# Performance work log

Hardware: AMD Instinct MI355X
Metric: run time of the kernel (lower is better)

Reference implementation:

```python
import jax, jax.numpy as jnp
import numpy as np

SHIFT = 1  # fixed realization of the random +/-1 shift_direction in __init__


def setup_inputs() -> dict:
    key = jax.random.key(0)
    k1, k2, k3 = jax.random.split(key, 3)
    x = jax.random.normal(k1, (1, 128, 56, 56), dtype=jnp.float32)
    w0 = jax.random.normal(k2, (32, 2, 3, 3), dtype=jnp.float32)   # weights[0]
    w1 = jax.random.normal(k3, (4, 64), dtype=jnp.float32)         # weights[1]
    return {"x": x, "w0": w0, "w1": w1}


def reference(x, w0, w1):
    # x: [1,128,56,56] -> [1,64,2,56,56]
    t3 = x.reshape(1, 64, 2, 56, 56)
    # 1x1 channel mix: contract the 64 axis with w1 [4,64]
    t4 = jnp.einsum('kjlmn,ij->kilmn', t3, w1)  # [1,4,2,56,56]
    # First unfold: kernel 3 along the last spatial axis (h2), zero pad 1.
    p1 = jnp.pad(t4, ((0, 0), (0, 0), (0, 0), (0, 0), (1, 1)))
    A = jnp.stack([p1[..., k:k + 56] for k in range(3)], axis=-2)  # [1,4,2,56,3,56]
    # Second unfold: kernel 3 along the SAME (already unfolded) position axis,
    # zero pad 1 applied to the unfolded tensor (matches torch's two-stage unfold).
    p2 = jnp.pad(A, ((0, 0), (0, 0), (0, 0), (0, 0), (0, 0), (1, 1)))
    B = jnp.stack([p2[..., k:k + 56] for k in range(3)], axis=-2)  # [1,4,2,56,3,3,56]
    # Contract group channel j=2 and both kernel offsets i,k with w0 [32,2,3,3]
    t6 = jnp.einsum('mpjoikn,ljik->mlpon', B, w0)  # [1,32,4,56,56]
    y = t6.reshape(1, 128, 56, 56)
    # Cyclic shift along H (axis 2)
    return jnp.roll(y, SHIFT, axis=2)
```

## Files before the change

### kernel.cpp

```cpp
#include <hip/hip_runtime.h>


__global__ __launch_bounds__(256) void fused_shift_unfold_kernel(
    const float* __restrict__ x,
    const float* __restrict__ w0,
    const float* __restrict__ w1,
    float* __restrict__ out)
{
    __shared__ float s_t4[2][60];
    __shared__ float s_w0[576];

    const int tid = threadIdx.x;
    const int h   = blockIdx.x;
    const int p   = blockIdx.y;
    const int o   = h ? h - 1 : 55;

    if (tid < 112) {
        const int j = (tid >= 56);
        const int n = tid - j * 56;
        const float* xp = x + j * 3136 + o * 56 + n;
        const float* wp = w1 + p * 64;
        float a0 = 0.f, a1 = 0.f, a2 = 0.f, a3 = 0.f;
        #pragma unroll
        for (int q = 0; q < 64; q += 4) {
            a0 += wp[q + 0] * xp[(q + 0) * 6272];
            a1 += wp[q + 1] * xp[(q + 1) * 6272];
            a2 += wp[q + 2] * xp[(q + 2) * 6272];
            a3 += wp[q + 3] * xp[(q + 3) * 6272];
        }
        s_t4[j][n + 2] = (a0 + a1) + (a2 + a3);
    } else {
        const int t = tid - 112;
        ((float4*)s_w0)[t] = ((const float4*)w0)[t];
        if (t < 8) {
            const int j   = t & 1;
            const int q2  = t >> 1;
            s_t4[j][q2 < 2 ? q2 : q2 + 56] = 0.f;
        }
    }
    __syncthreads();

    const int l = tid >> 3;
    const int b = tid & 7;

    float wreg[2][9];
    #pragma unroll
    for (int j = 0; j < 2; ++j)
        #pragma unroll
        for (int t = 0; t < 9; ++t)
            wreg[j][t] = s_w0[l * 18 + j * 9 + t];

    float* obase = out + (l * 4 + p) * 3136 + h * 56;
    #pragma unroll
    for (int i7 = 0; i7 < 7; ++i7) {
        const int n = b + i7 * 8;
        float acc = 0.f;
        #pragma unroll
        for (int k = 0; k < 3; ++k) {
            float s = 0.f;
            #pragma unroll
            for (int j = 0; j < 2; ++j) {
                const float* rp = &s_t4[j][n];
                s += wreg[j][0 + k] * rp[k + 0];
                s += wreg[j][3 + k] * rp[k + 1];
                s += wreg[j][6 + k] * rp[k + 2];
            }
            const int m = n + k - 1;
            acc += ((unsigned)m < 56u) ? s : 0.f;
        }
        obase[n] = acc;
    }
}

extern "C" void kernel_launch(void* const* d_in, const int* in_sizes, int n_in,
                              void* d_out, int out_size, void* d_ws, size_t ws_size,
                              hipStream_t stream) {
    (void)in_sizes; (void)n_in; (void)out_size; (void)d_ws; (void)ws_size;
    const float* x  = (const float*)d_in[0];
    const float* w0 = (const float*)d_in[1];
    const float* w1 = (const float*)d_in[2];
    float* out = (float*)d_out;

    dim3 grid(56, 4);
    fused_shift_unfold_kernel<<<grid, 256, 0, stream>>>(x, w0, w1, out);
}
```

Baseline: 59.37 us.

## Split channel reduction across thread pairs and vectorize output stores with float4

Doubles the block to 512 threads. Each 64-term channel reduction is now split across two lanes and combined with a shuffle, which halves the serial chain of strided global loads per thread. The output stage is reorganized so each thread computes 4 consecutive outputs from a register window and writes them with one float4 store, instead of 7 scalar stores. In exchange it adds a shuffle, leaves idle lanes (g>=14), and puts more threads per block.

Result: no change. 59.86 us (+0.8%).

```diff
diff --git a/kernel.cpp b/kernel.cpp
--- a/kernel.cpp
+++ b/kernel.cpp
@@ -1,7 +1,7 @@
 #include <hip/hip_runtime.h>
 
 
-__global__ __launch_bounds__(256) void fused_shift_unfold_kernel(
+__global__ __launch_bounds__(512) void fused_shift_unfold_kernel(
     const float* __restrict__ x,
     const float* __restrict__ w0,
     const float* __restrict__ w1,
@@ -15,60 +15,74 @@
     const int p   = blockIdx.y;
     const int o   = h ? h - 1 : 55;
 
-    if (tid < 112) {
-        const int j = (tid >= 56);
-        const int n = tid - j * 56;
-        const float* xp = x + j * 3136 + o * 56 + n;
-        const float* wp = w1 + p * 64;
+    if (tid < 224) {
+        const int v    = tid >> 1;
+        const int half = tid & 1;
+        const int j    = (v >= 56);
+        const int n    = v - j * 56;
+        const float* xp = x + j * 3136 + o * 56 + n + half * 32 * 6272;
+        const float* wp = w1 + p * 64 + half * 32;
         float a0 = 0.f, a1 = 0.f, a2 = 0.f, a3 = 0.f;
         #pragma unroll
-        for (int q = 0; q < 64; q += 4) {
+        for (int q = 0; q < 32; q += 4) {
             a0 += wp[q + 0] * xp[(q + 0) * 6272];
             a1 += wp[q + 1] * xp[(q + 1) * 6272];
             a2 += wp[q + 2] * xp[(q + 2) * 6272];
             a3 += wp[q + 3] * xp[(q + 3) * 6272];
         }
-        s_t4[j][n + 2] = (a0 + a1) + (a2 + a3);
-    } else {
-        const int t = tid - 112;
+        float a = (a0 + a1) + (a2 + a3);
+        float b = __shfl_xor(a, 1);
+        if (half == 0) s_t4[j][n + 2] = a + b;
+    } else if (tid < 368) {
+        const int t = tid - 224;
         ((float4*)s_w0)[t] = ((const float4*)w0)[t];
         if (t < 8) {
-            const int j   = t & 1;
-            const int q2  = t >> 1;
+            const int j  = t & 1;
+            const int q2 = t >> 1;
             s_t4[j][q2 < 2 ? q2 : q2 + 56] = 0.f;
         }
     }
     __syncthreads();
 
-    const int l = tid >> 3;
-    const int b = tid & 7;
+    const int g = tid & 15;
+    const int l = tid >> 4;
+    if (g < 14) {
+        float wreg[2][9];
+        #pragma unroll
+        for (int j = 0; j < 2; ++j)
+            #pragma unroll
+            for (int t = 0; t < 9; ++t)
+                wreg[j][t] = s_w0[l * 18 + j * 9 + t];
 
-    float wreg[2][9];
-    #pragma unroll
-    for (int j = 0; j < 2; ++j)
+        float r[2][8];
         #pragma unroll
-        for (int t = 0; t < 9; ++t)
-            wreg[j][t] = s_w0[l * 18 + j * 9 + t];
+        for (int j = 0; j < 2; ++j)
+            #pragma unroll
+            for (int d = 0; d < 8; ++d)
+                r[j][d] = s_t4[j][g * 4 + d];
 
-    float* obase = out + (l * 4 + p) * 3136 + h * 56;
-    #pragma unroll
-    for (int i7 = 0; i7 < 7; ++i7) {
-        const int n = b + i7 * 8;
-        float acc = 0.f;
+        float4 res;
+        float* rf = (float*)&res;
         #pragma unroll
-        for (int k = 0; k < 3; ++k) {
-            float s = 0.f;
+        for (int u = 0; u < 4; ++u) {
+            const int n = g * 4 + u;
+            float acc = 0.f;
             #pragma unroll
-            for (int j = 0; j < 2; ++j) {
-                const float* rp = &s_t4[j][n];
-                s += wreg[j][0 + k] * rp[k + 0];
-                s += wreg[j][3 + k] * rp[k + 1];
-                s += wreg[j][6 + k] * rp[k + 2];
+            for (int k = 0; k < 3; ++k) {
+                float s = 0.f;
+                #pragma unroll
+                for (int j = 0; j < 2; ++j) {
+                    s += wreg[j][0 + k] * r[j][u + k + 0];
+                    s += wreg[j][3 + k] * r[j][u + k + 1];
+                    s += wreg[j][6 + k] * r[j][u + k + 2];
+                }
+                const int m = n + k - 1;
+                acc += ((unsigned)m < 56u) ? s : 0.f;
             }
-            const int m = n + k - 1;
-            acc += ((unsigned)m < 56u) ? s : 0.f;
+            rf[u] = acc;
         }
-        obase[n] = acc;
+        float* obase = out + (l * 4 + p) * 3136 + h * 56 + g * 4;
+        *(float4*)obase = res;
     }
 }
 
@@ -82,5 +96,5 @@
     float* out = (float*)d_out;
 
     dim3 grid(56, 4);
-    fused_shift_unfold_kernel<<<grid, 256, 0, stream>>>(x, w0, w1, out);
+    fused_shift_unfold_kernel<<<grid, 512, 0, stream>>>(x, w0, w1, out);
 }
```
